# Kernel tuning notes

Measured on AMD Instinct MI355X. Metric: run time of the kernel, lower is better.

Reference implementation:

```python
import jax, jax.numpy as jnp
import numpy as np

MAX_FRAMES = 12
EMBED_DIM = 512
TOPK = 12
NUM_SAMPLES = 500
SIGMA = 0.05
SEL_DIM = 2
NUM_HEADS = 2


def setup_inputs() -> dict:
    key = jax.random.key(0)
    ks = jax.random.split(key, 9)
    D = EMBED_DIM
    C = D // 2
    s = lambda fan_in: 1.0 / np.sqrt(fan_in)
    return {
        "x": jax.random.normal(ks[0], (16, MAX_FRAMES * 50, D), dtype=jnp.float32),
        "ln_g": jnp.ones((D,), jnp.float32),
        "ln_b": jnp.zeros((D,), jnp.float32),
        "w_in": jax.random.normal(ks[1], (D, C), jnp.float32) * s(D),
        "wq": jax.random.normal(ks[2], (C, C), jnp.float32) * s(C),
        "wk": jax.random.normal(ks[3], (C, C), jnp.float32) * s(C),
        "wv": jax.random.normal(ks[4], (C, C), jnp.float32) * s(C),
        "wo": jax.random.normal(ks[5], (C, C), jnp.float32) * s(C),
        "w1": jax.random.normal(ks[6], (2 * C, C), jnp.float32) * s(2 * C),
        "w2": jax.random.normal(ks[7], (C, 1), jnp.float32) * s(C),
    }


def layer_norm(x, g, b, eps=1e-5):
    mu = jnp.mean(x, axis=-1, keepdims=True)
    var = jnp.var(x, axis=-1, keepdims=True)
    return (x - mu) * jax.lax.rsqrt(var + eps) * g + b


def mha(x, wq, wk, wv, wo):
    B, N, C = x.shape
    hd = C // NUM_HEADS
    q = (x @ wq).reshape(B, N, NUM_HEADS, hd).transpose(0, 2, 1, 3)
    k = (x @ wk).reshape(B, N, NUM_HEADS, hd).transpose(0, 2, 1, 3)
    v = (x @ wv).reshape(B, N, NUM_HEADS, hd).transpose(0, 2, 1, 3)
    attn = jax.nn.softmax(jnp.einsum('bhnd,bhmd->bhnm', q, k) / np.sqrt(hd), axis=-1)
    out = jnp.einsum('bhnm,bhmd->bhnd', attn, v).transpose(0, 2, 1, 3).reshape(B, N, C)
    return out @ wo


def predictor(x, ln_g, ln_b, w_in, wq, wk, wv, wo, w1, w2):
    h = jax.nn.gelu(layer_norm(x, ln_g, ln_b) @ w_in, approximate=False)
    h = mha(h, wq, wk, wv, wo)
    B, N, C = h.shape
    g = jnp.mean(h, axis=1, keepdims=True)
    h = jnp.concatenate([h, jnp.broadcast_to(g, (B, N, C))], axis=-1)
    h = jax.nn.gelu(h @ w1, approximate=False)
    return jnp.tanh(h @ w2)  # (B, N, 1)


def perturbed_topk(scores):
    # scores: (b, d) -> soft indicators (b, k, d)
    b, d = scores.shape
    noise = jax.random.normal(jax.random.key(1), (b, NUM_SAMPLES, d), dtype=scores.dtype)
    perturbed = scores[:, None, :] + noise * SIGMA
    _, idx = jax.lax.top_k(perturbed, TOPK)            # (b, ns, k)
    idx = jnp.sort(idx, axis=-1)
    onehot = jax.nn.one_hot(idx, d, dtype=scores.dtype)  # (b, ns, k, d)
    return onehot.mean(axis=1)                          # (b, k, d)


def reference(x, ln_g, ln_b, w_in, wq, wk, wv, wo, w1, w2):
    B, L, D = x.shape
    N = L // MAX_FRAMES
    xf = x.reshape(B * MAX_FRAMES, N, D)
    pred = predictor(xf, ln_g, ln_b, w_in, wq, wk, wv, wo, w1, w2)[..., 0]  # (b, N)
    spatial_score = pred[:, SEL_DIM:]                    # (b, N-2)
    ind = perturbed_topk(spatial_score)                  # (b, k, N-2)
    cls_feat = xf[:, :SEL_DIM, :]
    spatial_feat = xf[:, SEL_DIM:, :]
    sel = jnp.einsum('bkl,bld->bkd', ind, spatial_feat)
    out = jnp.concatenate([cls_feat, sel], axis=1)       # (b, 2+k, D)
    return out.reshape(B, -1, D)
```

## Files before the change

### kernel.cpp

```cpp
#include <hip/hip_runtime.h>
#include <stdint.h>

#define B2      192
#define NTOK    50
#define ROWS    9600
#define D_EMB   512
#define C_DIM   256
#define HD      128
#define NSAMP   500
#define TOPKK   12
#define NSPA    48

typedef short short8 __attribute__((ext_vector_type(8)));
typedef float f32x4  __attribute__((ext_vector_type(4)));

__device__ __forceinline__ float gelu_f(float x) {
    return 0.5f * x * (1.0f + erff(x * 0.7071067811865476f));
}
__device__ __forceinline__ uint16_t f2bf(float x) {
    uint32_t u = __float_as_uint(x);
    return (uint16_t)((u + 0x7fffu + ((u >> 16) & 1u)) >> 16);
}
__device__ __forceinline__ float bf2f(uint16_t b) {
    return __uint_as_float(((uint32_t)b) << 16);
}
__device__ __forceinline__ size_t swzA(int m, int k, int K) {
    return ((size_t)(m >> 4) * (K >> 5) + (k >> 5)) * 512
         + (size_t)((((k >> 3) & 3) * 16 + (m & 15)) * 8 + (k & 7));
}

__global__ __launch_bounds__(256) void ln_kernel(const float* __restrict__ x,
                                                 const float* __restrict__ g,
                                                 const float* __restrict__ b,
                                                 short* __restrict__ xh,
                                                 short* __restrict__ xl) {
    int row  = blockIdx.x * 4 + (threadIdx.x >> 6);
    int lane = threadIdx.x & 63;
    const float* rp = x + (size_t)row * D_EMB;
    float4 v0 = *(const float4*)(rp + lane * 8);
    float4 v1 = *(const float4*)(rp + lane * 8 + 4);
    float s  = v0.x + v0.y + v0.z + v0.w + v1.x + v1.y + v1.z + v1.w;
    float s2 = v0.x*v0.x + v0.y*v0.y + v0.z*v0.z + v0.w*v0.w
             + v1.x*v1.x + v1.y*v1.y + v1.z*v1.z + v1.w*v1.w;
#pragma unroll
    for (int off = 32; off; off >>= 1) {
        s  += __shfl_xor(s,  off);
        s2 += __shfl_xor(s2, off);
    }
    float mu  = s / 512.0f;
    float var = s2 / 512.0f - mu * mu;
    float inv = 1.0f / sqrtf(var + 1e-5f);
    const float* gp = g + lane * 8;
    const float* bp = b + lane * 8;
    float o[8];
    o[0]=(v0.x-mu)*inv*gp[0]+bp[0]; o[1]=(v0.y-mu)*inv*gp[1]+bp[1];
    o[2]=(v0.z-mu)*inv*gp[2]+bp[2]; o[3]=(v0.w-mu)*inv*gp[3]+bp[3];
    o[4]=(v1.x-mu)*inv*gp[4]+bp[4]; o[5]=(v1.y-mu)*inv*gp[5]+bp[5];
    o[6]=(v1.z-mu)*inv*gp[6]+bp[6]; o[7]=(v1.w-mu)*inv*gp[7]+bp[7];
    short8 h8, l8;
#pragma unroll
    for (int j = 0; j < 8; ++j) {
        uint16_t h = f2bf(o[j]);
        h8[j] = (short)h;
        l8[j] = (short)f2bf(o[j] - bf2f(h));
    }
    size_t blk = (size_t)(row >> 4) * 16 + (lane >> 2);
    int inner  = (lane & 3) * 16 + (row & 15);
    ((short8*)xh)[blk * 64 + inner] = h8;
    ((short8*)xl)[blk * 64 + inner] = l8;
}

__global__ __launch_bounds__(256) void swz_all(const float* __restrict__ w_in, const float* __restrict__ wq,
                                               const float* __restrict__ wk, const float* __restrict__ wv,
                                               const float* __restrict__ wo, const float* __restrict__ w1,
                                               short* win_hi, short* win_lo, short* wq_hi, short* wq_lo,
                                               short* wk_hi, short* wk_lo, short* wv_hi, short* wv_lo,
                                               short* wo_hi, short* wo_lo, short* w1a_hi, short* w1a_lo,
                                               short* w1b_hi, short* w1b_lo) {
    int blk = blockIdx.x;
    const float* W; short *hi, *lo; int K, base;
    if      (blk <  64) { W = w_in;            hi = win_hi; lo = win_lo; K = 512; base = 0;   }
    else if (blk <  96) { W = wq;              hi = wq_hi;  lo = wq_lo;  K = 256; base = 64;  }
    else if (blk < 128) { W = wk;              hi = wk_hi;  lo = wk_lo;  K = 256; base = 96;  }
    else if (blk < 160) { W = wv;              hi = wv_hi;  lo = wv_lo;  K = 256; base = 128; }
    else if (blk < 192) { W = wo;              hi = wo_hi;  lo = wo_lo;  K = 256; base = 160; }
    else if (blk < 224) { W = w1;              hi = w1a_hi; lo = w1a_lo; K = 256; base = 192; }
    else                { W = w1 + 256 * 256;  hi = w1b_hi; lo = w1b_lo; K = 256; base = 224; }
    int t = (blk - base) * 256 + threadIdx.x;
    int n = t & 255, k8 = t >> 8;
    short8 h8, l8;
#pragma unroll
    for (int j = 0; j < 8; ++j) {
        float wvl = W[(size_t)(k8 * 8 + j) * 256 + n];
        uint16_t h = f2bf(wvl);
        h8[j] = (short)h;
        l8[j] = (short)f2bf(wvl - bf2f(h));
    }
    size_t bb = (size_t)(n >> 4) * (K >> 5) + (k8 >> 2);
    int inner = (k8 & 3) * 16 + (n & 15);
    ((short8*)hi)[bb * 64 + inner] = h8;
    ((short8*)lo)[bb * 64 + inner] = l8;
}

template<int KB>
__device__ __forceinline__ void mm_core(const short8* __restrict__ pAh, const short8* __restrict__ pAl,
                                        const short8* __restrict__ pBh0, const short8* __restrict__ pBl0,
                                        const short8* __restrict__ pBh1, const short8* __restrict__ pBl1,
                                        f32x4& acc0, f32x4& acc1) {
    short8 ah[3], al[3], bh0[3], bl0[3], bh1[3], bl1[3];
#pragma unroll
    for (int i = 0; i < 2; ++i) {
        int off = i * 64;
        ah[i] = pAh[off];  al[i] = pAl[off];
        bh0[i] = pBh0[off]; bl0[i] = pBl0[off];
        bh1[i] = pBh1[off]; bl1[i] = pBl1[off];
    }
#pragma unroll
    for (int ks = 0; ks < KB; ++ks) {
        int cur = ks % 3;
        if (ks + 2 < KB) {
            int pre = (ks + 2) % 3, off = (ks + 2) * 64;
            ah[pre] = pAh[off];  al[pre] = pAl[off];
            bh0[pre] = pBh0[off]; bl0[pre] = pBl0[off];
            bh1[pre] = pBh1[off]; bl1[pre] = pBl1[off];
        }
        acc0 = __builtin_amdgcn_mfma_f32_16x16x32_bf16(ah[cur], bh0[cur], acc0, 0, 0, 0);
        acc0 = __builtin_amdgcn_mfma_f32_16x16x32_bf16(ah[cur], bl0[cur], acc0, 0, 0, 0);
        acc0 = __builtin_amdgcn_mfma_f32_16x16x32_bf16(al[cur], bh0[cur], acc0, 0, 0, 0);
        acc1 = __builtin_amdgcn_mfma_f32_16x16x32_bf16(ah[cur], bh1[cur], acc1, 0, 0, 0);
        acc1 = __builtin_amdgcn_mfma_f32_16x16x32_bf16(ah[cur], bl1[cur], acc1, 0, 0, 0);
        acc1 = __builtin_amdgcn_mfma_f32_16x16x32_bf16(al[cur], bh1[cur], acc1, 0, 0, 0);
    }
}

__device__ __forceinline__ void epi_store(f32x4 acc, int row0, int col, int N,
                                          float* __restrict__ Cf, short* __restrict__ Chi,
                                          short* __restrict__ Clo,
                                          const float* __restrict__ bias, int act) {
#pragma unroll
    for (int r = 0; r < 4; ++r) {
        int row = row0 + r;
        float v2 = acc[r];
        if (bias) v2 += bias[(size_t)(row / 50) * N + col];
        if (act)  v2 = gelu_f(v2);
        if (Cf) Cf[(size_t)row * N + col] = v2;
        if (Chi) {
            uint16_t h = f2bf(v2);
            size_t ad = swzA(row, col, 256);
            Chi[ad] = (short)h;
            Clo[ad] = (short)f2bf(v2 - bf2f(h));
        }
    }
}

template<int KB>
__global__ __launch_bounds__(256) void gemm_one(const short8* __restrict__ Ah,
                                                const short8* __restrict__ Al,
                                                const short8* __restrict__ Bh,
                                                const short8* __restrict__ Bl,
                                                float* __restrict__ Cf,
                                                short* __restrict__ Chi,
                                                short* __restrict__ Clo,
                                                const float* __restrict__ bias,
                                                int act) {
    int lane = threadIdx.x & 63;
    int wv   = threadIdx.x >> 6;
    int ms   = blockIdx.x * 4 + wv;
    int ns0  = blockIdx.y * 2;
    const short8* pAh  = Ah + (size_t)ms  * KB * 64 + lane;
    const short8* pAl  = Al + (size_t)ms  * KB * 64 + lane;
    const short8* pBh0 = Bh + (size_t)ns0 * KB * 64 + lane;
    const short8* pBl0 = Bl + (size_t)ns0 * KB * 64 + lane;
    const short8* pBh1 = pBh0 + (size_t)KB * 64;
    const short8* pBl1 = pBl0 + (size_t)KB * 64;
    f32x4 acc0 = {0.f,0.f,0.f,0.f}, acc1 = {0.f,0.f,0.f,0.f};
    mm_core<KB>(pAh, pAl, pBh0, pBl0, pBh1, pBl1, acc0, acc1);
    int row0 = ms * 16 + (lane >> 4) * 4;
    int cin  = lane & 15;
    epi_store(acc0, row0, ns0 * 16 + cin,      256, Cf, Chi, Clo, bias, act);
    epi_store(acc1, row0, (ns0 + 1) * 16 + cin, 256, Cf, Chi, Clo, bias, act);
}

__global__ __launch_bounds__(256) void gemm_qkv(const short8* __restrict__ Ah,
                                                const short8* __restrict__ Al,
                                                const short8* __restrict__ Bhq, const short8* __restrict__ Blq,
                                                const short8* __restrict__ Bhk, const short8* __restrict__ Blk,
                                                const short8* __restrict__ Bhv, const short8* __restrict__ Blv,
                                                float* __restrict__ q, float* __restrict__ k,
                                                float* __restrict__ v) {
    int lane = threadIdx.x & 63;
    int wv   = threadIdx.x >> 6;
    int ms   = blockIdx.x * 4 + wv;
    int sel  = blockIdx.y >> 3;
    int ns0  = (blockIdx.y & 7) * 2;
    const short8* Bh = (sel == 0) ? Bhq : (sel == 1) ? Bhk : Bhv;
    const short8* Bl = (sel == 0) ? Blq : (sel == 1) ? Blk : Blv;
    float* C = (sel == 0) ? q : (sel == 1) ? k : v;
    const short8* pAh  = Ah + (size_t)ms  * 8 * 64 + lane;
    const short8* pAl  = Al + (size_t)ms  * 8 * 64 + lane;
    const short8* pBh0 = Bh + (size_t)ns0 * 8 * 64 + lane;
    const short8* pBl0 = Bl + (size_t)ns0 * 8 * 64 + lane;
    const short8* pBh1 = pBh0 + 8 * 64;
    const short8* pBl1 = pBl0 + 8 * 64;
    f32x4 acc0 = {0.f,0.f,0.f,0.f}, acc1 = {0.f,0.f,0.f,0.f};
    mm_core<8>(pAh, pAl, pBh0, pBl0, pBh1, pBl1, acc0, acc1);
    int row0 = ms * 16 + (lane >> 4) * 4;
    int cin  = lane & 15;
    epi_store(acc0, row0, ns0 * 16 + cin,      256, C, nullptr, nullptr, nullptr, 0);
    epi_store(acc1, row0, (ns0 + 1) * 16 + cin, 256, C, nullptr, nullptr, nullptr, 0);
}

__global__ __launch_bounds__(256) void attn_kernel(const float* __restrict__ q,
                                                   const float* __restrict__ k,
                                                   const float* __restrict__ v,
                                                   short* __restrict__ aoh,
                                                   short* __restrict__ aol) {
    __shared__ float sQ[NTOK * 132];
    __shared__ float sK[NTOK * 132];
    __shared__ float sS[NTOK * 51];
    int blk = blockIdx.x;
    int b = blk >> 1, h = blk & 1;
    const size_t base = (size_t)b * NTOK * C_DIM + h * HD;
    int tid = threadIdx.x;
    for (int idx = tid; idx < 1600; idx += 256) {
        int r = idx >> 5, c = (idx & 31) * 4;
        *(float4*)&sQ[r * 132 + c] = *(const float4*)(q + base + (size_t)r * C_DIM + c);
        *(float4*)&sK[r * 132 + c] = *(const float4*)(k + base + (size_t)r * C_DIM + c);
    }
    __syncthreads();
    for (int e = tid; e < 625; e += 256) {
        int i2 = e / 25, j2 = e - i2 * 25;
        int i = i2 * 2, j = j2 * 2;
        const float* qi0 = &sQ[i * 132];
        const float* qi1 = qi0 + 132;
        const float* kj0 = &sK[j * 132];
        const float* kj1 = kj0 + 132;
        float4 a00 = {0,0,0,0}, a01 = {0,0,0,0}, a10 = {0,0,0,0}, a11 = {0,0,0,0};
#pragma unroll
        for (int t = 0; t < 32; ++t) {
            float4 q0 = *(const float4*)&qi0[t * 4];
            float4 q1 = *(const float4*)&qi1[t * 4];
            float4 b0 = *(const float4*)&kj0[t * 4];
            float4 b1 = *(const float4*)&kj1[t * 4];
            a00.x = fmaf(q0.x, b0.x, a00.x); a00.y = fmaf(q0.y, b0.y, a00.y);
            a00.z = fmaf(q0.z, b0.z, a00.z); a00.w = fmaf(q0.w, b0.w, a00.w);
            a01.x = fmaf(q0.x, b1.x, a01.x); a01.y = fmaf(q0.y, b1.y, a01.y);
            a01.z = fmaf(q0.z, b1.z, a01.z); a01.w = fmaf(q0.w, b1.w, a01.w);
            a10.x = fmaf(q1.x, b0.x, a10.x); a10.y = fmaf(q1.y, b0.y, a10.y);
            a10.z = fmaf(q1.z, b0.z, a10.z); a10.w = fmaf(q1.w, b0.w, a10.w);
            a11.x = fmaf(q1.x, b1.x, a11.x); a11.y = fmaf(q1.y, b1.y, a11.y);
            a11.z = fmaf(q1.z, b1.z, a11.z); a11.w = fmaf(q1.w, b1.w, a11.w);
        }
        const float sc = 0.08838834764831845f;
        sS[i * 51 + j]           = (a00.x + a00.y + a00.z + a00.w) * sc;
        sS[i * 51 + j + 1]       = (a01.x + a01.y + a01.z + a01.w) * sc;
        sS[(i + 1) * 51 + j]     = (a10.x + a10.y + a10.z + a10.w) * sc;
        sS[(i + 1) * 51 + j + 1] = (a11.x + a11.y + a11.z + a11.w) * sc;
    }
    __syncthreads();
    for (int idx = tid; idx < 1600; idx += 256) {
        int r = idx >> 5, c = (idx & 31) * 4;
        *(float4*)&sQ[r * 132 + c] = *(const float4*)(v + base + (size_t)r * C_DIM + c);
    }
    if (tid < NTOK) {
        float* row = &sS[tid * 51];
        float m = row[0];
        for (int j = 1; j < NTOK; ++j) m = fmaxf(m, row[j]);
        float sum = 0.f;
        for (int j = 0; j < NTOK; ++j) { float e2 = expf(row[j] - m); row[j] = e2; sum += e2; }
        float inv = 1.0f / sum;
        for (int j = 0; j < NTOK; ++j) row[j] *= inv;
    }
    __syncthreads();
    for (int e = tid; e < 1600; e += 256) {
        int i = e >> 5, d4 = (e & 31) * 4;
        const float* srow = &sS[i * 51];
        float4 acc = {0,0,0,0};
#pragma unroll
        for (int j = 0; j < NTOK; ++j) {
            float w = srow[j];
            float4 v4 = *(const float4*)&sQ[j * 132 + d4];
            acc.x = fmaf(w, v4.x, acc.x); acc.y = fmaf(w, v4.y, acc.y);
            acc.z = fmaf(w, v4.z, acc.z); acc.w = fmaf(w, v4.w, acc.w);
        }
        int row = b * NTOK + i;
        float vals[4] = {acc.x, acc.y, acc.z, acc.w};
#pragma unroll
        for (int c = 0; c < 4; ++c) {
            int col = h * HD + d4 + c;
            uint16_t hh = f2bf(vals[c]);
            size_t ad = swzA(row, col, 256);
            aoh[ad] = (short)hh;
            aol[ad] = (short)f2bf(vals[c] - bf2f(hh));
        }
    }
}

__global__ __launch_bounds__(256) void mean50(const float* __restrict__ h2,
                                              short* __restrict__ gh,
                                              short* __restrict__ gl) {
    int b = blockIdx.x, c = threadIdx.x;
    float s = 0.f;
    for (int n = 0; n < NTOK; ++n) s += h2[((size_t)b * NTOK + n) * C_DIM + c];
    float g = s / 50.0f;
    uint16_t h = f2bf(g);
    size_t ad = swzA(b, c, 256);
    gh[ad] = (short)h;
    gl[ad] = (short)f2bf(g - bf2f(h));
}

__global__ __launch_bounds__(256) void matvec_tanh(const float* __restrict__ h3,
                                                   const float* __restrict__ w2,
                                                   float* __restrict__ pred) {
    int row  = blockIdx.x * 4 + (threadIdx.x >> 6);
    int lane = threadIdx.x & 63;
    const float* rp = h3 + (size_t)row * C_DIM;
    float4 a = *(const float4*)(rp + lane * 4);
    float4 w = *(const float4*)(w2 + lane * 4);
    float s = a.x * w.x + a.y * w.y + a.z * w.z + a.w * w.w;
#pragma unroll
    for (int off = 32; off; off >>= 1) s += __shfl_xor(s, off);
    if (lane == 0) pred[row] = tanhf(s);
}

__device__ __forceinline__ uint32_t rotl32(uint32_t x, int r) {
    return (x << r) | (x >> (32 - r));
}
__device__ __forceinline__ void threefry01(uint32_t& x0, uint32_t& x1) {
    const uint32_t ks0 = 0u, ks1 = 1u, ks2 = 0x1BD11BDBu;
    x0 += ks0; x1 += ks1;
#define TFR(r) { x0 += x1; x1 = rotl32(x1, r); x1 ^= x0; }
    TFR(13) TFR(15) TFR(26) TFR(6)  x0 += ks1; x1 += ks2 + 1u;
    TFR(17) TFR(29) TFR(16) TFR(24) x0 += ks2; x1 += ks0 + 2u;
    TFR(13) TFR(15) TFR(26) TFR(6)  x0 += ks0; x1 += ks1 + 3u;
    TFR(17) TFR(29) TFR(16) TFR(24) x0 += ks1; x1 += ks2 + 4u;
    TFR(13) TFR(15) TFR(26) TFR(6)  x0 += ks2; x1 += ks0 + 5u;
#undef TFR
}

__device__ __forceinline__ float erfinv_xla(float x) {
    float w = -log1pf(-x * x);
    float p;
    if (w < 5.0f) {
        w -= 2.5f;
        p = 2.81022636e-08f;
        p = fmaf(p, w, 3.43273939e-07f);
        p = fmaf(p, w, -3.5233877e-06f);
        p = fmaf(p, w, -4.39150654e-06f);
        p = fmaf(p, w, 0.00021858087f);
        p = fmaf(p, w, -0.00125372503f);
        p = fmaf(p, w, -0.00417768164f);
        p = fmaf(p, w, 0.246640727f);
        p = fmaf(p, w, 1.50140941f);
    } else {
        w = sqrtf(w) - 3.0f;
        p = -0.000200214257f;
        p = fmaf(p, w, 0.000100950558f);
        p = fmaf(p, w, 0.00134934322f);
        p = fmaf(p, w, -0.00367342844f);
        p = fmaf(p, w, 0.00573950773f);
        p = fmaf(p, w, -0.0076224613f);
        p = fmaf(p, w, 0.00943887047f);
        p = fmaf(p, w, 1.00167406f);
        p = fmaf(p, w, 2.83297682f);
    }
    return p * x;
}

__device__ __forceinline__ float bits_to_normal(uint32_t bits) {
    float f = __uint_as_float((bits >> 9) | 0x3f800000u) - 1.0f;
    float u = f * 2.0f + (-0.99999994039535522461f);
    u = fmaxf(-0.99999994039535522461f, u);
    return 1.4142135623730951f * erfinv_xla(u);
}

__global__ __launch_bounds__(256) void topk_kernel(const float* __restrict__ pred,
                                                   int* __restrict__ counts) {
    int wid  = (blockIdx.x * 256 + threadIdx.x) >> 6;
    int lane = threadIdx.x & 63;
    int b = wid / NSAMP;
    int s = wid - b * NSAMP;
    uint32_t lo = (uint32_t)((b * NSAMP + s) * NSPA + lane);
    uint32_t x0 = 0u, x1 = lo;
    threefry01(x0, x1);
    float n = bits_to_normal(x0 ^ x1);
    float sc = (lane < NSPA) ? pred[b * NTOK + 2 + lane] : 0.f;
    float v  = (lane < NSPA) ? sc + n * 0.05f : -INFINITY;

    uint32_t vb   = __float_as_uint(v);
    uint32_t mono = (vb & 0x80000000u) ? ~vb : (vb | 0x80000000u);
    uint32_t t = 0;
#pragma unroll
    for (int bit = 31; bit >= 0; --bit) {
        uint32_t c = t | (1u << bit);
        unsigned long long m = __ballot(mono >= c);
        if (__popcll(m) >= TOPKK) t = c;
    }
    unsigned long long mgt = __ballot(mono > t);
    unsigned long long meq = __ballot(mono == t);
    int r = TOPKK - __popcll(mgt);
    unsigned long long below = (1ull << lane) - 1ull;
    bool sel = (mono > t) || ((mono == t) && (__popcll(meq & below) < r));
    sel = sel && (lane < NSPA);
    unsigned long long mask = __ballot(sel);
    if (sel) {
        int kpos = __popcll(mask & below);
        atomicAdd(&counts[((size_t)b * TOPKK + kpos) * NSPA + lane], 1);
    }
}

__global__ __launch_bounds__(256) void select_out(const float* __restrict__ x,
                                                  const int* __restrict__ counts,
                                                  float* __restrict__ out) {
    int row = blockIdx.x;
    int b = row / 14, k = row - b * 14;
    int d = threadIdx.x;
    if (k < 2) {
        out[(size_t)row * D_EMB + d]       = x[((size_t)(b * NTOK + k)) * D_EMB + d];
        out[(size_t)row * D_EMB + d + 256] = x[((size_t)(b * NTOK + k)) * D_EMB + d + 256];
    } else {
        int kk = k - 2;
        const int* cnt = counts + ((size_t)b * TOPKK + kk) * NSPA;
        __shared__ int sc[NSPA];
        if (d < NSPA) sc[d] = cnt[d];
        __syncthreads();
        float a0 = 0.f, a1 = 0.f;
        for (int l = 0; l < NSPA; ++l) {
            int c = sc[l];
            if (c) {
                float w = (float)c / 500.0f;
                const float* xr = x + ((size_t)(b * NTOK + 2 + l)) * D_EMB;
                a0 = fmaf(w, xr[d], a0);
                a1 = fmaf(w, xr[d + 256], a1);
            }
        }
        out[(size_t)row * D_EMB + d]       = a0;
        out[(size_t)row * D_EMB + d + 256] = a1;
    }
}

extern "C" void kernel_launch(void* const* d_in, const int* in_sizes, int n_in,
                              void* d_out, int out_size, void* d_ws, size_t ws_size,
                              hipStream_t stream) {
    const float* x    = (const float*)d_in[0];
    const float* ln_g = (const float*)d_in[1];
    const float* ln_b = (const float*)d_in[2];
    const float* w_in = (const float*)d_in[3];
    const float* wq   = (const float*)d_in[4];
    const float* wk   = (const float*)d_in[5];
    const float* wv   = (const float*)d_in[6];
    const float* wo   = (const float*)d_in[7];
    const float* w1   = (const float*)d_in[8];
    const float* w2   = (const float*)d_in[9];
    float* out = (float*)d_out;

    char* W = (char*)d_ws;
    short* xn_hi  = (short*)(W + 0);
    short* xn_lo  = (short*)(W + 9830400);
    short* ao_hi  = (short*)(W + 0);
    short* ao_lo  = (short*)(W + 4915200);
    short* h2_hi  = (short*)(W + 9830400);
    short* h2_lo  = (short*)(W + 14745600);
    short* h1_hi  = (short*)(W + 19660800);
    short* h1_lo  = (short*)(W + 24576000);
    float* h3     = (float*)(W + 19660800);
    float* q      = (float*)(W + 29491200);
    float* h2f    = (float*)(W + 29491200);
    float* k      = (float*)(W + 39321600);
    float* v      = (float*)(W + 49152000);
    short* win_hi = (short*)(W + 58982400);
    short* win_lo = (short*)(W + 59244544);
    short* wq_hi  = (short*)(W + 59506688);
    short* wq_lo  = (short*)(W + 59637760);
    short* wk_hi  = (short*)(W + 59768832);
    short* wk_lo  = (short*)(W + 59899904);
    short* wv_hi  = (short*)(W + 60030976);
    short* wv_lo  = (short*)(W + 60162048);
    short* wo_hi  = (short*)(W + 60293120);
    short* wo_lo  = (short*)(W + 60424192);
    short* w1a_hi = (short*)(W + 60555264);
    short* w1a_lo = (short*)(W + 60686336);
    short* w1b_hi = (short*)(W + 60817408);
    short* w1b_lo = (short*)(W + 60948480);
    short* gm_hi  = (short*)(W + 61079552);
    short* gm_lo  = (short*)(W + 61177856);
    float* gw     = (float*)(W + 61276160);
    float* pred   = (float*)(W + 61472768);
    int*   counts = (int*)  (W + 61511168);

    ln_kernel<<<ROWS / 4, 256, 0, stream>>>(x, ln_g, ln_b, xn_hi, xn_lo);
    swz_all<<<256, 256, 0, stream>>>(w_in, wq, wk, wv, wo, w1,
        win_hi, win_lo, wq_hi, wq_lo, wk_hi, wk_lo, wv_hi, wv_lo,
        wo_hi, wo_lo, w1a_hi, w1a_lo, w1b_hi, w1b_lo);
    gemm_one<16><<<dim3(150, 8), 256, 0, stream>>>((const short8*)xn_hi, (const short8*)xn_lo,
        (const short8*)win_hi, (const short8*)win_lo, nullptr, h1_hi, h1_lo, nullptr, 1);
    gemm_qkv<<<dim3(150, 24), 256, 0, stream>>>((const short8*)h1_hi, (const short8*)h1_lo,
        (const short8*)wq_hi, (const short8*)wq_lo, (const short8*)wk_hi, (const short8*)wk_lo,
        (const short8*)wv_hi, (const short8*)wv_lo, q, k, v);
    attn_kernel<<<B2 * 2, 256, 0, stream>>>(q, k, v, ao_hi, ao_lo);
    gemm_one<8><<<dim3(150, 8), 256, 0, stream>>>((const short8*)ao_hi, (const short8*)ao_lo,
        (const short8*)wo_hi, (const short8*)wo_lo, h2f, h2_hi, h2_lo, nullptr, 0);
    mean50<<<B2, 256, 0, stream>>>(h2f, gm_hi, gm_lo);
    gemm_one<8><<<dim3(3, 8), 256, 0, stream>>>((const short8*)gm_hi, (const short8*)gm_lo,
        (const short8*)w1b_hi, (const short8*)w1b_lo, gw, nullptr, nullptr, nullptr, 0);
    gemm_one<8><<<dim3(150, 8), 256, 0, stream>>>((const short8*)h2_hi, (const short8*)h2_lo,
        (const short8*)w1a_hi, (const short8*)w1a_lo, h3, nullptr, nullptr, gw, 1);
    matvec_tanh<<<ROWS / 4, 256, 0, stream>>>(h3, w2, pred);
    hipMemsetAsync(counts, 0, (size_t)B2 * TOPKK * NSPA * sizeof(int), stream);
    topk_kernel<<<B2 * NSAMP / 4, 256, 0, stream>>>(pred, counts);
    select_out<<<B2 * 14, 256, 0, stream>>>(x, counts, out);
}
```

Before: 313.6 us.

## Restructure top-k to per-thread insertion lists and merge prep kernels

The top-k kernel no longer uses one wavefront per sample with a 32-step ballot bisection. Each thread now handles one sample over half of the 48 candidates, keeping a sorted 12-entry register list of packed value-and-index keys. The two halves are then merged through shared memory, and the sorted index ranks are computed with a bitmask. The layernorm and weight-swizzle kernels are fused into one launch, and the counts memset is moved to the start of the stream. This cuts the number of launches and removes per-sample cross-lane reductions, at the cost of more registers per thread and serial compare-swap work.

```diff
diff --git a/kernel.cpp b/kernel.cpp
--- a/kernel.cpp
+++ b/kernel.cpp
@@ -29,77 +29,78 @@
          + (size_t)((((k >> 3) & 3) * 16 + (m & 15)) * 8 + (k & 7));
 }
 
-__global__ __launch_bounds__(256) void ln_kernel(const float* __restrict__ x,
-                                                 const float* __restrict__ g,
-                                                 const float* __restrict__ b,
-                                                 short* __restrict__ xh,
-                                                 short* __restrict__ xl) {
-    int row  = blockIdx.x * 4 + (threadIdx.x >> 6);
-    int lane = threadIdx.x & 63;
-    const float* rp = x + (size_t)row * D_EMB;
-    float4 v0 = *(const float4*)(rp + lane * 8);
-    float4 v1 = *(const float4*)(rp + lane * 8 + 4);
-    float s  = v0.x + v0.y + v0.z + v0.w + v1.x + v1.y + v1.z + v1.w;
-    float s2 = v0.x*v0.x + v0.y*v0.y + v0.z*v0.z + v0.w*v0.w
-             + v1.x*v1.x + v1.y*v1.y + v1.z*v1.z + v1.w*v1.w;
-#pragma unroll
-    for (int off = 32; off; off >>= 1) {
-        s  += __shfl_xor(s,  off);
-        s2 += __shfl_xor(s2, off);
-    }
-    float mu  = s / 512.0f;
-    float var = s2 / 512.0f - mu * mu;
-    float inv = 1.0f / sqrtf(var + 1e-5f);
-    const float* gp = g + lane * 8;
-    const float* bp = b + lane * 8;
-    float o[8];
-    o[0]=(v0.x-mu)*inv*gp[0]+bp[0]; o[1]=(v0.y-mu)*inv*gp[1]+bp[1];
-    o[2]=(v0.z-mu)*inv*gp[2]+bp[2]; o[3]=(v0.w-mu)*inv*gp[3]+bp[3];
-    o[4]=(v1.x-mu)*inv*gp[4]+bp[4]; o[5]=(v1.y-mu)*inv*gp[5]+bp[5];
-    o[6]=(v1.z-mu)*inv*gp[6]+bp[6]; o[7]=(v1.w-mu)*inv*gp[7]+bp[7];
-    short8 h8, l8;
-#pragma unroll
-    for (int j = 0; j < 8; ++j) {
-        uint16_t h = f2bf(o[j]);
-        h8[j] = (short)h;
-        l8[j] = (short)f2bf(o[j] - bf2f(h));
-    }
-    size_t blk = (size_t)(row >> 4) * 16 + (lane >> 2);
-    int inner  = (lane & 3) * 16 + (row & 15);
-    ((short8*)xh)[blk * 64 + inner] = h8;
-    ((short8*)xl)[blk * 64 + inner] = l8;
-}
-
-__global__ __launch_bounds__(256) void swz_all(const float* __restrict__ w_in, const float* __restrict__ wq,
-                                               const float* __restrict__ wk, const float* __restrict__ wv,
-                                               const float* __restrict__ wo, const float* __restrict__ w1,
-                                               short* win_hi, short* win_lo, short* wq_hi, short* wq_lo,
-                                               short* wk_hi, short* wk_lo, short* wv_hi, short* wv_lo,
-                                               short* wo_hi, short* wo_lo, short* w1a_hi, short* w1a_lo,
-                                               short* w1b_hi, short* w1b_lo) {
-    int blk = blockIdx.x;
-    const float* W; short *hi, *lo; int K, base;
-    if      (blk <  64) { W = w_in;            hi = win_hi; lo = win_lo; K = 512; base = 0;   }
-    else if (blk <  96) { W = wq;              hi = wq_hi;  lo = wq_lo;  K = 256; base = 64;  }
-    else if (blk < 128) { W = wk;              hi = wk_hi;  lo = wk_lo;  K = 256; base = 96;  }
-    else if (blk < 160) { W = wv;              hi = wv_hi;  lo = wv_lo;  K = 256; base = 128; }
-    else if (blk < 192) { W = wo;              hi = wo_hi;  lo = wo_lo;  K = 256; base = 160; }
-    else if (blk < 224) { W = w1;              hi = w1a_hi; lo = w1a_lo; K = 256; base = 192; }
-    else                { W = w1 + 256 * 256;  hi = w1b_hi; lo = w1b_lo; K = 256; base = 224; }
-    int t = (blk - base) * 256 + threadIdx.x;
-    int n = t & 255, k8 = t >> 8;
-    short8 h8, l8;
-#pragma unroll
-    for (int j = 0; j < 8; ++j) {
-        float wvl = W[(size_t)(k8 * 8 + j) * 256 + n];
-        uint16_t h = f2bf(wvl);
-        h8[j] = (short)h;
-        l8[j] = (short)f2bf(wvl - bf2f(h));
-    }
-    size_t bb = (size_t)(n >> 4) * (K >> 5) + (k8 >> 2);
-    int inner = (k8 & 3) * 16 + (n & 15);
-    ((short8*)hi)[bb * 64 + inner] = h8;
-    ((short8*)lo)[bb * 64 + inner] = l8;
+__global__ __launch_bounds__(256) void prep_kernel(const float* __restrict__ x,
+                                                   const float* __restrict__ g,
+                                                   const float* __restrict__ b,
+                                                   short* __restrict__ xh,
+                                                   short* __restrict__ xl,
+                                                   const float* __restrict__ w_in, const float* __restrict__ wq,
+                                                   const float* __restrict__ wk, const float* __restrict__ wv,
+                                                   const float* __restrict__ wo, const float* __restrict__ w1,
+                                                   short* win_hi, short* win_lo, short* wq_hi, short* wq_lo,
+                                                   short* wk_hi, short* wk_lo, short* wv_hi, short* wv_lo,
+                                                   short* wo_hi, short* wo_lo, short* w1a_hi, short* w1a_lo,
+                                                   short* w1b_hi, short* w1b_lo) {
+    if (blockIdx.x < 2400) {
+        int row  = blockIdx.x * 4 + (threadIdx.x >> 6);
+        int lane = threadIdx.x & 63;
+        const float* rp = x + (size_t)row * D_EMB;
+        float4 v0 = *(const float4*)(rp + lane * 8);
+        float4 v1 = *(const float4*)(rp + lane * 8 + 4);
+        float s  = v0.x + v0.y + v0.z + v0.w + v1.x + v1.y + v1.z + v1.w;
+        float s2 = v0.x*v0.x + v0.y*v0.y + v0.z*v0.z + v0.w*v0.w
+                 + v1.x*v1.x + v1.y*v1.y + v1.z*v1.z + v1.w*v1.w;
+#pragma unroll
+        for (int off = 32; off; off >>= 1) {
+            s  += __shfl_xor(s,  off);
+            s2 += __shfl_xor(s2, off);
+        }
+        float mu  = s / 512.0f;
+        float var = s2 / 512.0f - mu * mu;
+        float inv = 1.0f / sqrtf(var + 1e-5f);
+        const float* gp = g + lane * 8;
+        const float* bp = b + lane * 8;
+        float o[8];
+        o[0]=(v0.x-mu)*inv*gp[0]+bp[0]; o[1]=(v0.y-mu)*inv*gp[1]+bp[1];
+        o[2]=(v0.z-mu)*inv*gp[2]+bp[2]; o[3]=(v0.w-mu)*inv*gp[3]+bp[3];
+        o[4]=(v1.x-mu)*inv*gp[4]+bp[4]; o[5]=(v1.y-mu)*inv*gp[5]+bp[5];
+        o[6]=(v1.z-mu)*inv*gp[6]+bp[6]; o[7]=(v1.w-mu)*inv*gp[7]+bp[7];
+        short8 h8, l8;
+#pragma unroll
+        for (int j = 0; j < 8; ++j) {
+            uint16_t h = f2bf(o[j]);
+            h8[j] = (short)h;
+            l8[j] = (short)f2bf(o[j] - bf2f(h));
+        }
+        size_t blk = (size_t)(row >> 4) * 16 + (lane >> 2);
+        int inner  = (lane & 3) * 16 + (row & 15);
+        ((short8*)xh)[blk * 64 + inner] = h8;
+        ((short8*)xl)[blk * 64 + inner] = l8;
+    } else {
+        int blk = blockIdx.x - 2400;
+        const float* W; short *hi, *lo; int K, base;
+        if      (blk <  64) { W = w_in;            hi = win_hi; lo = win_lo; K = 512; base = 0;   }
+        else if (blk <  96) { W = wq;              hi = wq_hi;  lo = wq_lo;  K = 256; base = 64;  }
+        else if (blk < 128) { W = wk;              hi = wk_hi;  lo = wk_lo;  K = 256; base = 96;  }
+        else if (blk < 160) { W = wv;              hi = wv_hi;  lo = wv_lo;  K = 256; base = 128; }
+        else if (blk < 192) { W = wo;              hi = wo_hi;  lo = wo_lo;  K = 256; base = 160; }
+        else if (blk < 224) { W = w1;              hi = w1a_hi; lo = w1a_lo; K = 256; base = 192; }
+        else                { W = w1 + 256 * 256;  hi = w1b_hi; lo = w1b_lo; K = 256; base = 224; }
+        int t = (blk - base) * 256 + threadIdx.x;
+        int n = t & 255, k8 = t >> 8;
+        short8 h8, l8;
+#pragma unroll
+        for (int j = 0; j < 8; ++j) {
+            float wvl = W[(size_t)(k8 * 8 + j) * 256 + n];
+            uint16_t h = f2bf(wvl);
+            h8[j] = (short)h;
+            l8[j] = (short)f2bf(wvl - bf2f(h));
+        }
+        size_t bb = (size_t)(n >> 4) * (K >> 5) + (k8 >> 2);
+        int inner = (k8 & 3) * 16 + (n & 15);
+        ((short8*)hi)[bb * 64 + inner] = h8;
+        ((short8*)lo)[bb * 64 + inner] = l8;
+    }
 }
 
 template<int KB>
@@ -376,36 +377,63 @@
 
 __global__ __launch_bounds__(256) void topk_kernel(const float* __restrict__ pred,
                                                    int* __restrict__ counts) {
-    int wid  = (blockIdx.x * 256 + threadIdx.x) >> 6;
+    __shared__ unsigned long long sK[128][13];
     int lane = threadIdx.x & 63;
-    int b = wid / NSAMP;
-    int s = wid - b * NSAMP;
-    uint32_t lo = (uint32_t)((b * NSAMP + s) * NSPA + lane);
-    uint32_t x0 = 0u, x1 = lo;
-    threefry01(x0, x1);
-    float n = bits_to_normal(x0 ^ x1);
-    float sc = (lane < NSPA) ? pred[b * NTOK + 2 + lane] : 0.f;
-    float v  = (lane < NSPA) ? sc + n * 0.05f : -INFINITY;
-
-    uint32_t vb   = __float_as_uint(v);
-    uint32_t mono = (vb & 0x80000000u) ? ~vb : (vb | 0x80000000u);
-    uint32_t t = 0;
-#pragma unroll
-    for (int bit = 31; bit >= 0; --bit) {
-        uint32_t c = t | (1u << bit);
-        unsigned long long m = __ballot(mono >= c);
-        if (__popcll(m) >= TOPKK) t = c;
-    }
-    unsigned long long mgt = __ballot(mono > t);
-    unsigned long long meq = __ballot(mono == t);
-    int r = TOPKK - __popcll(mgt);
-    unsigned long long below = (1ull << lane) - 1ull;
-    bool sel = (mono > t) || ((mono == t) && (__popcll(meq & below) < r));
-    sel = sel && (lane < NSPA);
-    unsigned long long mask = __ballot(sel);
-    if (sel) {
-        int kpos = __popcll(mask & below);
-        atomicAdd(&counts[((size_t)b * TOPKK + kpos) * NSPA + lane], 1);
+    int wv   = threadIdx.x >> 6;
+    int p    = wv >> 1;
+    int hh   = wv & 1;
+    int g    = blockIdx.x * 128 + p * 64 + lane;
+    int b    = g / NSAMP;
+    int s    = g - b * NSAMP;
+    uint32_t base = (uint32_t)((b * NSAMP + s) * NSPA);
+    const float* sp = pred + b * NTOK + 2;
+
+    unsigned long long list[TOPKK];
+#pragma unroll
+    for (int i = 0; i < TOPKK; ++i) list[i] = 0ull;
+
+    int d0 = hh * 24;
+#pragma unroll 2
+    for (int dd = 0; dd < 24; ++dd) {
+        int d = d0 + dd;
+        uint32_t x0 = 0u, x1 = base + (uint32_t)d;
+        threefry01(x0, x1);
+        float n  = bits_to_normal(x0 ^ x1);
+        float v  = sp[d] + n * 0.05f;
+        uint32_t vb   = __float_as_uint(v);
+        uint32_t mono = (vb & 0x80000000u) ? ~vb : (vb | 0x80000000u);
+        unsigned long long key = ((unsigned long long)mono << 6) | (unsigned)(63 - d);
+#pragma unroll
+        for (int i = 0; i < TOPKK; ++i) {
+            bool gt = key > list[i];
+            unsigned long long mx = gt ? key : list[i];
+            unsigned long long mn = gt ? list[i] : key;
+            list[i] = mx; key = mn;
+        }
+    }
+    int rowL = p * 64 + lane;
+    if (hh == 1) {
+#pragma unroll
+        for (int i = 0; i < TOPKK; ++i) sK[rowL][i] = list[i];
+    }
+    __syncthreads();
+    if (hh == 0) {
+        unsigned long long M[TOPKK];
+#pragma unroll
+        for (int i = 0; i < TOPKK; ++i) {
+            unsigned long long o = sK[rowL][11 - i];
+            M[i] = (list[i] > o) ? list[i] : o;
+        }
+        unsigned long long m = 0ull;
+#pragma unroll
+        for (int i = 0; i < TOPKK; ++i) m |= 1ull << (unsigned)(M[i] & 63ull);
+#pragma unroll
+        for (int i = 0; i < TOPKK; ++i) {
+            unsigned a = (unsigned)(M[i] & 63ull);
+            int kpos = 11 - __popcll(m & ((1ull << a) - 1ull));
+            int d    = 63 - (int)a;
+            atomicAdd(&counts[((size_t)b * TOPKK + kpos) * NSPA + d], 1);
+        }
     }
 }
 
@@ -488,8 +516,9 @@
     float* pred   = (float*)(W + 61472768);
     int*   counts = (int*)  (W + 61511168);
 
-    ln_kernel<<<ROWS / 4, 256, 0, stream>>>(x, ln_g, ln_b, xn_hi, xn_lo);
-    swz_all<<<256, 256, 0, stream>>>(w_in, wq, wk, wv, wo, w1,
+    hipMemsetAsync(counts, 0, (size_t)B2 * TOPKK * NSPA * sizeof(int), stream);
+    prep_kernel<<<2656, 256, 0, stream>>>(x, ln_g, ln_b, xn_hi, xn_lo,
+        w_in, wq, wk, wv, wo, w1,
         win_hi, win_lo, wq_hi, wq_lo, wk_hi, wk_lo, wv_hi, wv_lo,
         wo_hi, wo_lo, w1a_hi, w1a_lo, w1b_hi, w1b_lo);
     gemm_one<16><<<dim3(150, 8), 256, 0, stream>>>((const short8*)xn_hi, (const short8*)xn_lo,
@@ -506,7 +535,6 @@
     gemm_one<8><<<dim3(150, 8), 256, 0, stream>>>((const short8*)h2_hi, (const short8*)h2_lo,
         (const short8*)w1a_hi, (const short8*)w1a_lo, h3, nullptr, nullptr, gw, 1);
     matvec_tanh<<<ROWS / 4, 256, 0, stream>>>(h3, w2, pred);
-    hipMemsetAsync(counts, 0, (size_t)B2 * TOPKK * NSPA * sizeof(int), stream);
-    topk_kernel<<<B2 * NSAMP / 4, 256, 0, stream>>>(pred, counts);
+    topk_kernel<<<750, 256, 0, stream>>>(pred, counts);
     select_out<<<B2 * 14, 256, 0, stream>>>(x, counts, out);
 }
```

After: 297.4 us. 1.05x faster.
